# Optimization experiments

Measured on AMD Instinct MI355X. Metric: run time of the kernel, lower is better.

Reference implementation:

```python
import jax, jax.numpy as jnp
import numpy as np

B, C_IN, C_OUT, D, H, W = 2, 128, 128, 16, 32, 32


def setup_inputs() -> dict:
    key = jax.random.key(0)
    kx, kw, kb = jax.random.split(key, 3)
    x = jax.random.normal(kx, (B, C_IN, D, H, W), dtype=jnp.float32)
    # ddpm_conv3x3 -> Conv3d(in_ch, out_ch, kernel=3, padding=1) with default (scaled-variance) init
    fan_in = C_IN * 3 * 3 * 3
    scale = 1.0 / np.sqrt(fan_in)
    Wk = jax.random.uniform(kw, (C_OUT, C_IN, 3, 3, 3), dtype=jnp.float32, minval=-scale, maxval=scale)
    b = jnp.zeros((C_OUT,), dtype=jnp.float32)
    return {"x": x, "Wk": Wk, "b": b}


def reference(x, Wk, b):
    h = jnp.repeat(jnp.repeat(jnp.repeat(x, 2, axis=2), 2, axis=3), 2, axis=4)
    # 3x3x3 conv, stride 1, padding 1 (SAME)
    out = jax.lax.conv_general_dilated(
        h, Wk,
        window_strides=(1, 1, 1),
        padding="SAME",
        dimension_numbers=("NCDHW", "OIDHW", "NCDHW"),
    )
    return out + b[None, :, None, None, None]
```

## Files before the change

kernel.cpp:

```cpp
#include <hip/hip_runtime.h>
#include <hip/hip_bf16.h>

#define B_    2
#define CIN   128
#define COUT  128
#define DD    16
#define HH    32
#define WW    32
#define OS_H2 64
#define OS_D2 (64*64)
#define OS_CO (32*64*64)
#define OS_B  (COUT*OS_CO)

#define PD_D   18
#define PD_H   34
#define RD     17
#define RDB    68
#define HWDW   (PD_H*RD)
#define PLB    (HWDW*4)
#define CIW    (PD_D*HWDW)
#define CIB    (CIW*4)
#define CI8B   (8*CIB)
#define ARRD   ((size_t)B_*CIN*CIW)
#define ARRB   (ARRD*4)
#define AFOLD_BYTES (8*32*8*64*16)

typedef __attribute__((ext_vector_type(8))) short        short8;
typedef __attribute__((ext_vector_type(4))) float        floatx4;
typedef __attribute__((ext_vector_type(4))) unsigned int uint4v;

static __device__ __forceinline__ unsigned f2bf(float f) {
    union { __hip_bfloat16 h; unsigned short u; } cv;
    cv.h = __float2bfloat16(f);
    return (unsigned)cv.u;
}

__global__ __launch_bounds__(256) void fold_kernel(const float* __restrict__ Wk,
                                                   unsigned short* __restrict__ Afold) {
    const int t = blockIdx.x * 256 + threadIdx.x;
    const int p  = t >> 14;
    const int ks = (t >> 9) & 31;
    const int ct = (t >> 6) & 7;
    const int l  = t & 63;
    const int co = ct * 16 + (l & 15);
    const int ci = ks * 4 + (l >> 4);
    const int ed = (p >> 2) & 1, eh = (p >> 1) & 1, ew = p & 1;

    const float* w = Wk + (co * CIN + ci) * 27;
    float wv[27];
    #pragma unroll
    for (int i = 0; i < 27; ++i) wv[i] = w[i];

    short8 pk;
    #pragma unroll
    for (int tt = 0; tt < 8; ++tt) {
        const int td = (tt >> 2) & 1, th = (tt >> 1) & 1, tw = tt & 1;
        const int dlo = ed ? (td ? 2 : 0) : (td ? 1 : 0);
        const int dhi = ed ? (td ? 2 : 1) : (td ? 2 : 0);
        const int hlo = eh ? (th ? 2 : 0) : (th ? 1 : 0);
        const int hhi = eh ? (th ? 2 : 1) : (th ? 2 : 0);
        const int wlo = ew ? (tw ? 2 : 0) : (tw ? 1 : 0);
        const int whi = ew ? (tw ? 2 : 1) : (tw ? 2 : 0);
        float s = 0.f;
        for (int kd = dlo; kd <= dhi; ++kd)
            for (int kh = hlo; kh <= hhi; ++kh)
                for (int kw = wlo; kw <= whi; ++kw)
                    s += wv[kd * 9 + kh * 3 + kw];
        pk[tt] = (short)f2bf(s);
    }
    reinterpret_cast<short8*>(Afold)[t] = pk;
}

__global__ __launch_bounds__(256) void pad_kernel(const float* __restrict__ x,
                                                  unsigned* __restrict__ xe) {
    const int idx = blockIdx.x * 256 + threadIdx.x;
    const int w2 = idx & 15;
    const int h  = (idx >> 4) & 31;
    const int d  = (idx >> 9) & 15;
    const int ci = (idx >> 13) & 127;
    const int b  = (idx >> 20) & 1;
    const float2 v = *reinterpret_cast<const float2*>(
        x + (size_t)((b * CIN + ci) * DD + d) * (HH * WW) + h * WW + w2 * 2);
    xe[(size_t)((b * CIN + ci) * PD_D + d + 1) * HWDW
       + (h + 1) * RD + (w2 + 1)] = f2bf(v.x) | (f2bf(v.y) << 16);
}

__global__ __launch_bounds__(256) void xo_kernel(const unsigned* __restrict__ xe,
                                                 unsigned* __restrict__ xo) {
    const size_t t = (size_t)blockIdx.x * 256 + threadIdx.x;
    const unsigned e0 = xe[t];
    const unsigned e1 = (t + 1 < ARRD) ? xe[t + 1] : 0u;
    xo[t] = (e0 >> 16) | (e1 << 16);
}

__global__ __launch_bounds__(256, 3) void upconv_mfma(
    const char* __restrict__ xe_c, const char* __restrict__ xo_c,
    const unsigned short* __restrict__ Afold,
    const float* __restrict__ bias,
    float* __restrict__ out)
{
    __shared__ short Bt[2][128 * 64];
    char* buf0 = reinterpret_cast<char*>(&Bt[0][0]);
    char* buf1 = reinterpret_cast<char*>(&Bt[1][0]);

    const int tid  = threadIdx.x;
    const int wave = tid >> 6;
    const int lane = tid & 63;

    const int d      = blockIdx.x >> 3;
    const int h_base = (blockIdx.x & 7) * 4;
    const int p      = blockIdx.y;
    const int b      = blockIdx.z;
    const int ed = (p >> 2) & 1, eh = (p >> 1) & 1, ew = p & 1;

    const int npair = tid & 63;
    const int grp   = tid >> 6;
    const int hl    = npair >> 4;
    const int s     = npair & 15;
    const int n_a   = hl * 32 + 2 * s;
    const int n_b   = n_a + 1;
    const char* pa = ew ? xe_c : xo_c;
    const char* pb = ew ? xo_c : xe_c;
    const int dpad0 = d + ed;
    const int hpad0 = h_base + hl + eh;
    const long rowb = ((long)(b * CIN + grp * 2) * PD_D + dpad0) * (long)PLB
                    + (long)hpad0 * RDB;
    int offA[2], offB[2];
    offA[0] = (int)rowb + (s + ew) * 4;
    offB[0] = (int)rowb + (s + 1) * 4;
    offA[1] = offA[0] + CIB;
    offB[1] = offB[0] + CIB;

    int waddr_a[2], waddr_b[2];
    #pragma unroll
    for (int i = 0; i < 2; ++i) {
        const int cl = grp * 2 + i;
        waddr_a[i] = n_a * 128 + ((cl * 16) ^ (((n_a >> 1) & 7) << 4));
        waddr_b[i] = n_b * 128 + ((cl * 16) ^ (((n_b >> 1) & 7) << 4));
    }

    const int co0 = (wave >> 1) * 64;
    const int n0  = (wave & 1) * 64;
    const int ct0 = (wave >> 1) * 4;
    int raddr[2][4];
    #pragma unroll
    for (int ksl = 0; ksl < 2; ++ksl)
        #pragma unroll
        for (int nt = 0; nt < 4; ++nt) {
            const int n  = n0 + nt * 16 + (lane & 15);
            const int kb = ksl * 64 + (lane >> 4) * 16;
            raddr[ksl][nt] = n * 128 + (kb ^ (((n >> 1) & 7) << 4));
        }

    floatx4 acc[4][4];
    #pragma unroll
    for (int i = 0; i < 4; ++i)
        #pragma unroll
        for (int j = 0; j < 4; ++j)
            acc[i][j] = (floatx4){0.f, 0.f, 0.f, 0.f};

    const short8* Ap = reinterpret_cast<const short8*>(Afold);

    unsigned ga[2][4], gb[2][4];

    #define GATHER()                                                            \
        do {                                                                    \
            _Pragma("unroll")                                                   \
            for (int i = 0; i < 2; ++i) {                                       \
                const char* ba = pa + offA[i];                                  \
                const char* bb = pb + offB[i];                                  \
                ga[i][0] = *(const unsigned*)(ba + 0);                          \
                ga[i][1] = *(const unsigned*)(ba + RDB);                        \
                ga[i][2] = *(const unsigned*)(ba + PLB);                        \
                ga[i][3] = *(const unsigned*)(ba + PLB + RDB);                  \
                gb[i][0] = *(const unsigned*)(bb + 0);                          \
                gb[i][1] = *(const unsigned*)(bb + RDB);                        \
                gb[i][2] = *(const unsigned*)(bb + PLB);                        \
                gb[i][3] = *(const unsigned*)(bb + PLB + RDB);                  \
                offA[i] += CI8B; offB[i] += CI8B;                               \
            }                                                                   \
        } while (0)

    #define BODY(kc, bufc, dofill)                                              \
        do {                                                                    \
            short8 a[2][4];                                                     \
            _Pragma("unroll")                                                   \
            for (int ksl = 0; ksl < 2; ++ksl)                                   \
                _Pragma("unroll")                                               \
                for (int ct = 0; ct < 4; ++ct)                                  \
                    a[ksl][ct] = Ap[(size_t)(((p) * 32 + (kc) * 2 + ksl) * 8    \
                                             + ct0 + ct) * 64 + lane];          \
            _Pragma("unroll")                                                   \
            for (int i = 0; i < 2; ++i) {                                       \
                *(uint4v*)(bufc + waddr_a[i]) =                                 \
                    (uint4v){ga[i][0], ga[i][1], ga[i][2], ga[i][3]};           \
                *(uint4v*)(bufc + waddr_b[i]) =                                 \
                    (uint4v){gb[i][0], gb[i][1], gb[i][2], gb[i][3]};           \
            }                                                                   \
            if (dofill) GATHER();                                               \
            asm volatile("s_waitcnt lgkmcnt(0)\n\ts_barrier" ::: "memory");     \
            __builtin_amdgcn_s_setprio(1);                                      \
            _Pragma("unroll")                                                   \
            for (int ksl = 0; ksl < 2; ++ksl) {                                 \
                short8 bfr[4];                                                  \
                _Pragma("unroll")                                               \
                for (int nt = 0; nt < 4; ++nt)                                  \
                    bfr[nt] = *reinterpret_cast<const short8*>(                 \
                        (bufc) + raddr[ksl][nt]);                               \
                _Pragma("unroll")                                               \
                for (int ct = 0; ct < 4; ++ct)                                  \
                    _Pragma("unroll")                                           \
                    for (int nt = 0; nt < 4; ++nt)                              \
                        acc[ct][nt] = __builtin_amdgcn_mfma_f32_16x16x32_bf16(  \
                            a[ksl][ct], bfr[nt], acc[ct][nt], 0, 0, 0);         \
            }                                                                   \
            __builtin_amdgcn_s_setprio(0);                                      \
        } while (0)

    GATHER();
    for (int kc = 0; kc < 16; kc += 2) {
        BODY(kc,     buf0, true);
        BODY(kc + 1, buf1, (kc + 1) != 15);
    }
    #undef BODY
    #undef GATHER

    float* ob = out + (size_t)b * OS_B + (size_t)(2 * d + ed) * OS_D2;
    #pragma unroll
    for (int ct = 0; ct < 4; ++ct) {
        #pragma unroll
        for (int j = 0; j < 4; ++j) {
            const int co = co0 + ct * 16 + (lane >> 4) * 4 + j;
            const float bv = bias[co];
            #pragma unroll
            for (int nt = 0; nt < 4; ++nt) {
                const int n  = n0 + nt * 16 + (lane & 15);
                const int hh = n >> 5, wl = n & 31;
                const int h2 = 2 * (h_base + hh) + eh;
                const int w2 = 2 * wl + ew;
                ob[(size_t)co * OS_CO + h2 * OS_H2 + w2] = acc[ct][nt][j] + bv;
            }
        }
    }
}

extern "C" void kernel_launch(void* const* d_in, const int* in_sizes, int n_in,
                              void* d_out, int out_size, void* d_ws, size_t ws_size,
                              hipStream_t stream) {
    const float* x    = (const float*)d_in[0];
    const float* Wk   = (const float*)d_in[1];
    const float* bias = (const float*)d_in[2];
    float* out        = (float*)d_out;

    unsigned short* Afold = (unsigned short*)d_ws;
    char* xe = (char*)d_ws + AFOLD_BYTES;
    char* xo = xe + ARRB;

    hipMemsetAsync(xe, 0, ARRB, stream);
    pad_kernel<<<8192, 256, 0, stream>>>(x, (unsigned*)xe);
    xo_kernel<<<(unsigned)(ARRD / 256), 256, 0, stream>>>((const unsigned*)xe,
                                                          (unsigned*)xo);
    fold_kernel<<<512, 256, 0, stream>>>(Wk, Afold);

    dim3 grid(DD * 8, 8, B_);
    upconv_mfma<<<grid, 256, 0, stream>>>(xe, xo, Afold, bias, out);
}
```

Baseline: 115.9 us.

## Warp-specialize conv kernel with dedicated producer waves gathering into LDS

Adds two extra waves per block (384 threads) that only gather the padded bf16 input tiles from global memory and write them into the double-buffered LDS. The four MFMA waves now only prefetch weight fragments one step ahead and run matrix multiplies between barriers. The aim is to take global-gather latency and LDS-write work off the compute waves' critical path. In exchange the producer waves hold two in-flight gather sets, which raises register pressure and per-block resources. The barrier handshake between producer and consumer waves must also stay matched.

```diff
diff --git a/kernel.cpp b/kernel.cpp
--- a/kernel.cpp
+++ b/kernel.cpp
@@ -93,7 +93,7 @@
     xo[t] = (e0 >> 16) | (e1 << 16);
 }
 
-__global__ __launch_bounds__(256, 3) void upconv_mfma(
+__global__ __launch_bounds__(384, 3) void upconv_mfma(
     const char* __restrict__ xe_c, const char* __restrict__ xo_c,
     const unsigned short* __restrict__ Afold,
     const float* __restrict__ bias,
@@ -103,45 +103,90 @@
     char* buf0 = reinterpret_cast<char*>(&Bt[0][0]);
     char* buf1 = reinterpret_cast<char*>(&Bt[1][0]);
 
-    const int tid  = threadIdx.x;
-    const int wave = tid >> 6;
-    const int lane = tid & 63;
-
+    const int tid = threadIdx.x;
     const int d      = blockIdx.x >> 3;
     const int h_base = (blockIdx.x & 7) * 4;
     const int p      = blockIdx.y;
     const int b      = blockIdx.z;
     const int ed = (p >> 2) & 1, eh = (p >> 1) & 1, ew = p & 1;
 
-    const int npair = tid & 63;
-    const int grp   = tid >> 6;
-    const int hl    = npair >> 4;
-    const int s     = npair & 15;
-    const int n_a   = hl * 32 + 2 * s;
-    const int n_b   = n_a + 1;
-    const char* pa = ew ? xe_c : xo_c;
-    const char* pb = ew ? xo_c : xe_c;
-    const int dpad0 = d + ed;
-    const int hpad0 = h_base + hl + eh;
-    const long rowb = ((long)(b * CIN + grp * 2) * PD_D + dpad0) * (long)PLB
-                    + (long)hpad0 * RDB;
-    int offA[2], offB[2];
-    offA[0] = (int)rowb + (s + ew) * 4;
-    offB[0] = (int)rowb + (s + 1) * 4;
-    offA[1] = offA[0] + CIB;
-    offB[1] = offB[0] + CIB;
-
-    int waddr_a[2], waddr_b[2];
-    #pragma unroll
-    for (int i = 0; i < 2; ++i) {
-        const int cl = grp * 2 + i;
-        waddr_a[i] = n_a * 128 + ((cl * 16) ^ (((n_a >> 1) & 7) << 4));
-        waddr_b[i] = n_b * 128 + ((cl * 16) ^ (((n_b >> 1) & 7) << 4));
-    }
-
+    if (tid >= 256) {
+        const int ptid  = tid - 256;
+        const int npair = ptid & 63;
+        const int grp   = ptid >> 6;
+        const int hl    = npair >> 4;
+        const int s     = npair & 15;
+        const int n_a   = hl * 32 + 2 * s;
+        const int n_b   = n_a + 1;
+        const char* pa = ew ? xe_c : xo_c;
+        const char* pb = ew ? xo_c : xe_c;
+        const long rowb = ((long)(b * CIN + grp * 4) * PD_D + (d + ed)) * (long)PLB
+                        + (long)(h_base + hl + eh) * RDB;
+        int offA = (int)rowb + (s + ew) * 4;
+        int offB = (int)rowb + (s + 1) * 4;
+
+        int waddr_a[4], waddr_b[4];
+        #pragma unroll
+        for (int i = 0; i < 4; ++i) {
+            const int cl = grp * 4 + i;
+            waddr_a[i] = n_a * 128 + ((cl * 16) ^ (((n_a >> 1) & 7) << 4));
+            waddr_b[i] = n_b * 128 + ((cl * 16) ^ (((n_b >> 1) & 7) << 4));
+        }
+
+        unsigned gaA[4][4], gbA[4][4], gaB[4][4], gbB[4][4];
+
+        #define GATHERP(ga, gb)                                                 \
+            do {                                                                \
+                _Pragma("unroll")                                               \
+                for (int i = 0; i < 4; ++i) {                                   \
+                    const char* ba = pa + offA + i * CIB;                       \
+                    const char* bb = pb + offB + i * CIB;                       \
+                    ga[i][0] = *(const unsigned*)(ba + 0);                      \
+                    ga[i][1] = *(const unsigned*)(ba + RDB);                    \
+                    ga[i][2] = *(const unsigned*)(ba + PLB);                    \
+                    ga[i][3] = *(const unsigned*)(ba + PLB + RDB);              \
+                    gb[i][0] = *(const unsigned*)(bb + 0);                      \
+                    gb[i][1] = *(const unsigned*)(bb + RDB);                    \
+                    gb[i][2] = *(const unsigned*)(bb + PLB);                    \
+                    gb[i][3] = *(const unsigned*)(bb + PLB + RDB);              \
+                }                                                               \
+                offA += CI8B; offB += CI8B;                                     \
+            } while (0)
+
+        #define PWRITE(bufc, ga, gb)                                            \
+            do {                                                                \
+                _Pragma("unroll")                                               \
+                for (int i = 0; i < 4; ++i) {                                   \
+                    *(uint4v*)(bufc + waddr_a[i]) =                             \
+                        (uint4v){ga[i][0], ga[i][1], ga[i][2], ga[i][3]};       \
+                    *(uint4v*)(bufc + waddr_b[i]) =                             \
+                        (uint4v){gb[i][0], gb[i][1], gb[i][2], gb[i][3]};       \
+                }                                                               \
+            } while (0)
+
+        GATHERP(gaA, gbA);
+        GATHERP(gaB, gbB);
+        for (int kc = 0; kc < 16; kc += 2) {
+            PWRITE(buf0, gaA, gbA);
+            if (kc + 2 < 16) GATHERP(gaA, gbA);
+            asm volatile("s_waitcnt lgkmcnt(0)" ::: "memory");
+            __builtin_amdgcn_s_barrier();
+            PWRITE(buf1, gaB, gbB);
+            if (kc + 3 < 16) GATHERP(gaB, gbB);
+            asm volatile("s_waitcnt lgkmcnt(0)" ::: "memory");
+            __builtin_amdgcn_s_barrier();
+        }
+        #undef PWRITE
+        #undef GATHERP
+        return;
+    }
+
+    const int wave = tid >> 6;
+    const int lane = tid & 63;
     const int co0 = (wave >> 1) * 64;
     const int n0  = (wave & 1) * 64;
     const int ct0 = (wave >> 1) * 4;
+
     int raddr[2][4];
     #pragma unroll
     for (int ksl = 0; ksl < 2; ++ksl)
@@ -161,44 +206,20 @@
 
     const short8* Ap = reinterpret_cast<const short8*>(Afold);
 
-    unsigned ga[2][4], gb[2][4];
-
-    #define GATHER()                                                            \
+    short8 aC[2][4], aN[2][4];
+
+    #define ALOAD(a, kc)                                                        \
         do {                                                                    \
-            _Pragma("unroll")                                                   \
-            for (int i = 0; i < 2; ++i) {                                       \
-                const char* ba = pa + offA[i];                                  \
-                const char* bb = pb + offB[i];                                  \
-                ga[i][0] = *(const unsigned*)(ba + 0);                          \
-                ga[i][1] = *(const unsigned*)(ba + RDB);                        \
-                ga[i][2] = *(const unsigned*)(ba + PLB);                        \
-                ga[i][3] = *(const unsigned*)(ba + PLB + RDB);                  \
-                gb[i][0] = *(const unsigned*)(bb + 0);                          \
-                gb[i][1] = *(const unsigned*)(bb + RDB);                        \
-                gb[i][2] = *(const unsigned*)(bb + PLB);                        \
-                gb[i][3] = *(const unsigned*)(bb + PLB + RDB);                  \
-                offA[i] += CI8B; offB[i] += CI8B;                               \
-            }                                                                   \
-        } while (0)
-
-    #define BODY(kc, bufc, dofill)                                              \
-        do {                                                                    \
-            short8 a[2][4];                                                     \
             _Pragma("unroll")                                                   \
             for (int ksl = 0; ksl < 2; ++ksl)                                   \
                 _Pragma("unroll")                                               \
                 for (int ct = 0; ct < 4; ++ct)                                  \
                     a[ksl][ct] = Ap[(size_t)(((p) * 32 + (kc) * 2 + ksl) * 8    \
                                              + ct0 + ct) * 64 + lane];          \
-            _Pragma("unroll")                                                   \
-            for (int i = 0; i < 2; ++i) {                                       \
-                *(uint4v*)(bufc + waddr_a[i]) =                                 \
-                    (uint4v){ga[i][0], ga[i][1], ga[i][2], ga[i][3]};           \
-                *(uint4v*)(bufc + waddr_b[i]) =                                 \
-                    (uint4v){gb[i][0], gb[i][1], gb[i][2], gb[i][3]};           \
-            }                                                                   \
-            if (dofill) GATHER();                                               \
-            asm volatile("s_waitcnt lgkmcnt(0)\n\ts_barrier" ::: "memory");     \
+        } while (0)
+
+    #define MFMABLOCK(bufc, a)                                                  \
+        do {                                                                    \
             __builtin_amdgcn_s_setprio(1);                                      \
             _Pragma("unroll")                                                   \
             for (int ksl = 0; ksl < 2; ++ksl) {                                 \
@@ -217,13 +238,17 @@
             __builtin_amdgcn_s_setprio(0);                                      \
         } while (0)
 
-    GATHER();
+    ALOAD(aC, 0);
     for (int kc = 0; kc < 16; kc += 2) {
-        BODY(kc,     buf0, true);
-        BODY(kc + 1, buf1, (kc + 1) != 15);
-    }
-    #undef BODY
-    #undef GATHER
+        ALOAD(aN, kc + 1);
+        __builtin_amdgcn_s_barrier();
+        MFMABLOCK(buf0, aC);
+        if (kc + 2 < 16) ALOAD(aC, kc + 2);
+        __builtin_amdgcn_s_barrier();
+        MFMABLOCK(buf1, aN);
+    }
+    #undef MFMABLOCK
+    #undef ALOAD
 
     float* ob = out + (size_t)b * OS_B + (size_t)(2 * d + ed) * OS_D2;
     #pragma unroll
@@ -263,5 +288,5 @@
     fold_kernel<<<512, 256, 0, stream>>>(Wk, Afold);
 
     dim3 grid(DD * 8, 8, B_);
-    upconv_mfma<<<grid, 256, 0, stream>>>(xe, xo, Afold, bias, out);
-}
+    upconv_mfma<<<grid, 384, 0, stream>>>(xe, xo, Afold, bias, out);
+}
```

After: 182.0 us. +56.9%, slower.

## Double the spatial tile per block to reuse folded weights across more outputs

Applied to the files above, without the earlier changes.

Each block now covers 8 output rows (256 spatial positions) instead of 4. Each wave computes a 64x128 tile with 4x8 accumulators, so every A-fragment load from the folded weights serves twice as many MFMAs, and the grid is halved. In exchange, LDS per block doubles to 64KB, accumulator registers double, and launch bounds drop to 2 blocks per CU. The grid falls to 1024 blocks, which lowers occupancy and the scheduler's ability to hide latency.

```diff
diff --git a/kernel.cpp b/kernel.cpp
--- a/kernel.cpp
+++ b/kernel.cpp
@@ -93,13 +93,13 @@
     xo[t] = (e0 >> 16) | (e1 << 16);
 }
 
-__global__ __launch_bounds__(256, 3) void upconv_mfma(
+__global__ __launch_bounds__(256, 2) void upconv_mfma(
     const char* __restrict__ xe_c, const char* __restrict__ xo_c,
     const unsigned short* __restrict__ Afold,
     const float* __restrict__ bias,
     float* __restrict__ out)
 {
-    __shared__ short Bt[2][128 * 64];
+    __shared__ short Bt[2][256 * 64];
     char* buf0 = reinterpret_cast<char*>(&Bt[0][0]);
     char* buf1 = reinterpret_cast<char*>(&Bt[1][0]);
 
@@ -107,68 +107,63 @@
     const int wave = tid >> 6;
     const int lane = tid & 63;
 
-    const int d      = blockIdx.x >> 3;
-    const int h_base = (blockIdx.x & 7) * 4;
+    const int d      = blockIdx.x >> 2;
+    const int h_base = (blockIdx.x & 3) * 8;
     const int p      = blockIdx.y;
     const int b      = blockIdx.z;
     const int ed = (p >> 2) & 1, eh = (p >> 1) & 1, ew = p & 1;
 
-    const int npair = tid & 63;
-    const int grp   = tid >> 6;
+    const int npair = tid & 127;
+    const int cig   = tid >> 7;
     const int hl    = npair >> 4;
     const int s     = npair & 15;
     const int n_a   = hl * 32 + 2 * s;
     const int n_b   = n_a + 1;
     const char* pa = ew ? xe_c : xo_c;
     const char* pb = ew ? xo_c : xe_c;
-    const int dpad0 = d + ed;
-    const int hpad0 = h_base + hl + eh;
-    const long rowb = ((long)(b * CIN + grp * 2) * PD_D + dpad0) * (long)PLB
-                    + (long)hpad0 * RDB;
-    int offA[2], offB[2];
-    offA[0] = (int)rowb + (s + ew) * 4;
-    offB[0] = (int)rowb + (s + 1) * 4;
-    offA[1] = offA[0] + CIB;
-    offB[1] = offB[0] + CIB;
-
-    int waddr_a[2], waddr_b[2];
-    #pragma unroll
-    for (int i = 0; i < 2; ++i) {
-        const int cl = grp * 2 + i;
+    const long rowb = ((long)(b * CIN + cig * 4) * PD_D + (d + ed)) * (long)PLB
+                    + (long)(h_base + hl + eh) * RDB;
+    int offA = (int)rowb + (s + ew) * 4;
+    int offB = (int)rowb + (s + 1) * 4;
+
+    int waddr_a[4], waddr_b[4];
+    #pragma unroll
+    for (int i = 0; i < 4; ++i) {
+        const int cl = cig * 4 + i;
         waddr_a[i] = n_a * 128 + ((cl * 16) ^ (((n_a >> 1) & 7) << 4));
         waddr_b[i] = n_b * 128 + ((cl * 16) ^ (((n_b >> 1) & 7) << 4));
     }
 
-    const int co0 = (wave >> 1) * 64;
-    const int n0  = (wave & 1) * 64;
-    const int ct0 = (wave >> 1) * 4;
-    int raddr[2][4];
+    const int co0   = (wave >> 1) * 64;
+    const int nbase = (wave & 1) * 128;
+    const int ct0   = (wave >> 1) * 4;
+    int raddr[2][8];
     #pragma unroll
     for (int ksl = 0; ksl < 2; ++ksl)
         #pragma unroll
-        for (int nt = 0; nt < 4; ++nt) {
-            const int n  = n0 + nt * 16 + (lane & 15);
+        for (int nt = 0; nt < 8; ++nt) {
+            const int n  = nbase + nt * 16 + (lane & 15);
             const int kb = ksl * 64 + (lane >> 4) * 16;
             raddr[ksl][nt] = n * 128 + (kb ^ (((n >> 1) & 7) << 4));
         }
 
-    floatx4 acc[4][4];
+    floatx4 acc[4][8];
     #pragma unroll
     for (int i = 0; i < 4; ++i)
         #pragma unroll
-        for (int j = 0; j < 4; ++j)
+        for (int j = 0; j < 8; ++j)
             acc[i][j] = (floatx4){0.f, 0.f, 0.f, 0.f};
 
     const short8* Ap = reinterpret_cast<const short8*>(Afold);
 
-    unsigned ga[2][4], gb[2][4];
+    unsigned ga[4][4], gb[4][4];
 
     #define GATHER()                                                            \
         do {                                                                    \
             _Pragma("unroll")                                                   \
-            for (int i = 0; i < 2; ++i) {                                       \
-                const char* ba = pa + offA[i];                                  \
-                const char* bb = pb + offB[i];                                  \
+            for (int i = 0; i < 4; ++i) {                                       \
+                const char* ba = pa + offA + i * CIB;                           \
+                const char* bb = pb + offB + i * CIB;                           \
                 ga[i][0] = *(const unsigned*)(ba + 0);                          \
                 ga[i][1] = *(const unsigned*)(ba + RDB);                        \
                 ga[i][2] = *(const unsigned*)(ba + PLB);                        \
@@ -177,8 +172,8 @@
                 gb[i][1] = *(const unsigned*)(bb + RDB);                        \
                 gb[i][2] = *(const unsigned*)(bb + PLB);                        \
                 gb[i][3] = *(const unsigned*)(bb + PLB + RDB);                  \
-                offA[i] += CI8B; offB[i] += CI8B;                               \
             }                                                                   \
+            offA += CI8B; offB += CI8B;                                         \
         } while (0)
 
     #define BODY(kc, bufc, dofill)                                              \
@@ -191,7 +186,7 @@
                     a[ksl][ct] = Ap[(size_t)(((p) * 32 + (kc) * 2 + ksl) * 8    \
                                              + ct0 + ct) * 64 + lane];          \
             _Pragma("unroll")                                                   \
-            for (int i = 0; i < 2; ++i) {                                       \
+            for (int i = 0; i < 4; ++i) {                                       \
                 *(uint4v*)(bufc + waddr_a[i]) =                                 \
                     (uint4v){ga[i][0], ga[i][1], ga[i][2], ga[i][3]};           \
                 *(uint4v*)(bufc + waddr_b[i]) =                                 \
@@ -202,17 +197,15 @@
             __builtin_amdgcn_s_setprio(1);                                      \
             _Pragma("unroll")                                                   \
             for (int ksl = 0; ksl < 2; ++ksl) {                                 \
-                short8 bfr[4];                                                  \
                 _Pragma("unroll")                                               \
-                for (int nt = 0; nt < 4; ++nt)                                  \
-                    bfr[nt] = *reinterpret_cast<const short8*>(                 \
+                for (int nt = 0; nt < 8; ++nt) {                                \
+                    const short8 bfr = *reinterpret_cast<const short8*>(        \
                         (bufc) + raddr[ksl][nt]);                               \
-                _Pragma("unroll")                                               \
-                for (int ct = 0; ct < 4; ++ct)                                  \
                     _Pragma("unroll")                                           \
-                    for (int nt = 0; nt < 4; ++nt)                              \
+                    for (int ct = 0; ct < 4; ++ct)                              \
                         acc[ct][nt] = __builtin_amdgcn_mfma_f32_16x16x32_bf16(  \
-                            a[ksl][ct], bfr[nt], acc[ct][nt], 0, 0, 0);         \
+                            a[ksl][ct], bfr, acc[ct][nt], 0, 0, 0);             \
+                }                                                               \
             }                                                                   \
             __builtin_amdgcn_s_setprio(0);                                      \
         } while (0)
@@ -233,8 +226,8 @@
             const int co = co0 + ct * 16 + (lane >> 4) * 4 + j;
             const float bv = bias[co];
             #pragma unroll
-            for (int nt = 0; nt < 4; ++nt) {
-                const int n  = n0 + nt * 16 + (lane & 15);
+            for (int nt = 0; nt < 8; ++nt) {
+                const int n  = nbase + nt * 16 + (lane & 15);
                 const int hh = n >> 5, wl = n & 31;
                 const int h2 = 2 * (h_base + hh) + eh;
                 const int w2 = 2 * wl + ew;
@@ -262,6 +255,6 @@
                                                           (unsigned*)xo);
     fold_kernel<<<512, 256, 0, stream>>>(Wk, Afold);
 
-    dim3 grid(DD * 8, 8, B_);
+    dim3 grid(DD * 4, 8, B_);
     upconv_mfma<<<grid, 256, 0, stream>>>(xe, xo, Afold, bias, out);
 }
```

After: 125.9 us. +8.6%, slower.

## Load B fragments directly from global into registers, dropping LDS staging

Applied to the files above, without the earlier changes.

Removes the shared-memory staging buffer and barriers. Each lane now gathers its own MFMA B-operand fragment straight from the padded even/odd bf16 arrays into registers, with a two-deep register double buffer for both A and B. Occupancy drops from 3 to 2 blocks per SIMD target to make room for the extra registers. This avoids LDS writes, reads and workgroup syncs, but each wave now issues redundant global gathers (two waves share the same B data) and register pressure rises.

```diff
diff --git a/kernel.cpp b/kernel.cpp
--- a/kernel.cpp
+++ b/kernel.cpp
@@ -20,7 +20,6 @@
 #define PLB    (HWDW*4)
 #define CIW    (PD_D*HWDW)
 #define CIB    (CIW*4)
-#define CI8B   (8*CIB)
 #define ARRD   ((size_t)B_*CIN*CIW)
 #define ARRB   (ARRD*4)
 #define AFOLD_BYTES (8*32*8*64*16)
@@ -29,10 +28,10 @@
 typedef __attribute__((ext_vector_type(4))) float        floatx4;
 typedef __attribute__((ext_vector_type(4))) unsigned int uint4v;
 
-static __device__ __forceinline__ unsigned f2bf(float f) {
+static __device__ __forceinline__ unsigned short f2bf(float f) {
     union { __hip_bfloat16 h; unsigned short u; } cv;
     cv.h = __float2bfloat16(f);
-    return (unsigned)cv.u;
+    return cv.u;
 }
 
 __global__ __launch_bounds__(256) void fold_kernel(const float* __restrict__ Wk,
@@ -82,7 +81,7 @@
     const float2 v = *reinterpret_cast<const float2*>(
         x + (size_t)((b * CIN + ci) * DD + d) * (HH * WW) + h * WW + w2 * 2);
     xe[(size_t)((b * CIN + ci) * PD_D + d + 1) * HWDW
-       + (h + 1) * RD + (w2 + 1)] = f2bf(v.x) | (f2bf(v.y) << 16);
+       + (h + 1) * RD + (w2 + 1)] = (unsigned)f2bf(v.x) | ((unsigned)f2bf(v.y) << 16);
 }
 
 __global__ __launch_bounds__(256) void xo_kernel(const unsigned* __restrict__ xe,
@@ -93,16 +92,12 @@
     xo[t] = (e0 >> 16) | (e1 << 16);
 }
 
-__global__ __launch_bounds__(256, 3) void upconv_mfma(
+__global__ __launch_bounds__(256, 2) void upconv_mfma(
     const char* __restrict__ xe_c, const char* __restrict__ xo_c,
     const unsigned short* __restrict__ Afold,
     const float* __restrict__ bias,
     float* __restrict__ out)
 {
-    __shared__ short Bt[2][128 * 64];
-    char* buf0 = reinterpret_cast<char*>(&Bt[0][0]);
-    char* buf1 = reinterpret_cast<char*>(&Bt[1][0]);
-
     const int tid  = threadIdx.x;
     const int wave = tid >> 6;
     const int lane = tid & 63;
@@ -113,44 +108,18 @@
     const int b      = blockIdx.z;
     const int ed = (p >> 2) & 1, eh = (p >> 1) & 1, ew = p & 1;
 
-    const int npair = tid & 63;
-    const int grp   = tid >> 6;
-    const int hl    = npair >> 4;
-    const int s     = npair & 15;
-    const int n_a   = hl * 32 + 2 * s;
-    const int n_b   = n_a + 1;
-    const char* pa = ew ? xe_c : xo_c;
-    const char* pb = ew ? xo_c : xe_c;
-    const int dpad0 = d + ed;
-    const int hpad0 = h_base + hl + eh;
-    const long rowb = ((long)(b * CIN + grp * 2) * PD_D + dpad0) * (long)PLB
-                    + (long)hpad0 * RDB;
-    int offA[2], offB[2];
-    offA[0] = (int)rowb + (s + ew) * 4;
-    offB[0] = (int)rowb + (s + 1) * 4;
-    offA[1] = offA[0] + CIB;
-    offB[1] = offB[0] + CIB;
-
-    int waddr_a[2], waddr_b[2];
-    #pragma unroll
-    for (int i = 0; i < 2; ++i) {
-        const int cl = grp * 2 + i;
-        waddr_a[i] = n_a * 128 + ((cl * 16) ^ (((n_a >> 1) & 7) << 4));
-        waddr_b[i] = n_b * 128 + ((cl * 16) ^ (((n_b >> 1) & 7) << 4));
-    }
-
     const int co0 = (wave >> 1) * 64;
     const int n0  = (wave & 1) * 64;
     const int ct0 = (wave >> 1) * 4;
-    int raddr[2][4];
-    #pragma unroll
-    for (int ksl = 0; ksl < 2; ++ksl)
-        #pragma unroll
-        for (int nt = 0; nt < 4; ++nt) {
-            const int n  = n0 + nt * 16 + (lane & 15);
-            const int kb = ksl * 64 + (lane >> 4) * 16;
-            raddr[ksl][nt] = n * 128 + (kb ^ (((n >> 1) & 7) << 4));
-        }
+
+    const int lodd = lane & 1;
+    const char* arr = (ew != lodd) ? xe_c : xo_c;
+    const int ci_l  = lane >> 4;
+    const int col0  = ((lane & 15) >> 1) + (lodd ? 1 : ew);
+    const char* bbase = arr
+        + ((long)(b * CIN + ci_l) * PD_D + (d + ed)) * (long)PLB
+        + (long)(h_base + eh + (n0 >> 5)) * RDB
+        + (long)col0 * 4;
 
     floatx4 acc[4][4];
     #pragma unroll
@@ -161,69 +130,66 @@
 
     const short8* Ap = reinterpret_cast<const short8*>(Afold);
 
-    unsigned ga[2][4], gb[2][4];
-
-    #define GATHER()                                                            \
+    uint4v B0[2][4], B1[2][4];
+    short8 A0[2][4], A1[2][4];
+
+    #define LOADB(Bf, kc)                                                       \
         do {                                                                    \
             _Pragma("unroll")                                                   \
-            for (int i = 0; i < 2; ++i) {                                       \
-                const char* ba = pa + offA[i];                                  \
-                const char* bb = pb + offB[i];                                  \
-                ga[i][0] = *(const unsigned*)(ba + 0);                          \
-                ga[i][1] = *(const unsigned*)(ba + RDB);                        \
-                ga[i][2] = *(const unsigned*)(ba + PLB);                        \
-                ga[i][3] = *(const unsigned*)(ba + PLB + RDB);                  \
-                gb[i][0] = *(const unsigned*)(bb + 0);                          \
-                gb[i][1] = *(const unsigned*)(bb + RDB);                        \
-                gb[i][2] = *(const unsigned*)(bb + PLB);                        \
-                gb[i][3] = *(const unsigned*)(bb + PLB + RDB);                  \
-                offA[i] += CI8B; offB[i] += CI8B;                               \
-            }                                                                   \
+            for (int ksl = 0; ksl < 2; ++ksl)                                   \
+                _Pragma("unroll")                                               \
+                for (int nt = 0; nt < 4; ++nt) {                                \
+                    const char* fb = bbase + (long)((kc) * 8 + ksl * 4) * CIB   \
+                                   + (nt >> 1) * RDB + (nt & 1) * 32;           \
+                    Bf[ksl][nt] = (uint4v){                                     \
+                        *(const unsigned*)(fb),                                 \
+                        *(const unsigned*)(fb + RDB),                           \
+                        *(const unsigned*)(fb + PLB),                           \
+                        *(const unsigned*)(fb + PLB + RDB)};                    \
+                }                                                               \
         } while (0)
 
-    #define BODY(kc, bufc, dofill)                                              \
+    #define LOADA(Af, kc)                                                       \
         do {                                                                    \
-            short8 a[2][4];                                                     \
             _Pragma("unroll")                                                   \
             for (int ksl = 0; ksl < 2; ++ksl)                                   \
                 _Pragma("unroll")                                               \
                 for (int ct = 0; ct < 4; ++ct)                                  \
-                    a[ksl][ct] = Ap[(size_t)(((p) * 32 + (kc) * 2 + ksl) * 8    \
-                                             + ct0 + ct) * 64 + lane];          \
-            _Pragma("unroll")                                                   \
-            for (int i = 0; i < 2; ++i) {                                       \
-                *(uint4v*)(bufc + waddr_a[i]) =                                 \
-                    (uint4v){ga[i][0], ga[i][1], ga[i][2], ga[i][3]};           \
-                *(uint4v*)(bufc + waddr_b[i]) =                                 \
-                    (uint4v){gb[i][0], gb[i][1], gb[i][2], gb[i][3]};           \
-            }                                                                   \
-            if (dofill) GATHER();                                               \
-            asm volatile("s_waitcnt lgkmcnt(0)\n\ts_barrier" ::: "memory");     \
+                    Af[ksl][ct] = Ap[(size_t)(((p) * 32 + (kc) * 2 + ksl) * 8   \
+                                              + ct0 + ct) * 64 + lane];         \
+        } while (0)
+
+    #define MFMAC(Af, Bf)                                                       \
+        do {                                                                    \
             __builtin_amdgcn_s_setprio(1);                                      \
             _Pragma("unroll")                                                   \
-            for (int ksl = 0; ksl < 2; ++ksl) {                                 \
-                short8 bfr[4];                                                  \
+            for (int ksl = 0; ksl < 2; ++ksl)                                   \
                 _Pragma("unroll")                                               \
-                for (int nt = 0; nt < 4; ++nt)                                  \
-                    bfr[nt] = *reinterpret_cast<const short8*>(                 \
-                        (bufc) + raddr[ksl][nt]);                               \
-                _Pragma("unroll")                                               \
-                for (int ct = 0; ct < 4; ++ct)                                  \
+                for (int nt = 0; nt < 4; ++nt) {                                \
+                    const short8 bfr = __builtin_bit_cast(short8, Bf[ksl][nt]); \
                     _Pragma("unroll")                                           \
-                    for (int nt = 0; nt < 4; ++nt)                              \
+                    for (int ct = 0; ct < 4; ++ct)                              \
                         acc[ct][nt] = __builtin_amdgcn_mfma_f32_16x16x32_bf16(  \
-                            a[ksl][ct], bfr[nt], acc[ct][nt], 0, 0, 0);         \
-            }                                                                   \
+                            Af[ksl][ct], bfr, acc[ct][nt], 0, 0, 0);            \
+                }                                                               \
             __builtin_amdgcn_s_setprio(0);                                      \
         } while (0)
 
-    GATHER();
+    LOADB(B0, 0);
+    LOADA(A0, 0);
     for (int kc = 0; kc < 16; kc += 2) {
-        BODY(kc,     buf0, true);
-        BODY(kc + 1, buf1, (kc + 1) != 15);
+        LOADB(B1, kc + 1);
+        LOADA(A1, kc + 1);
+        MFMAC(A0, B0);
+        if (kc + 2 < 16) {
+            LOADB(B0, kc + 2);
+            LOADA(A0, kc + 2);
+        }
+        MFMAC(A1, B1);
     }
-    #undef BODY
-    #undef GATHER
+    #undef MFMAC
+    #undef LOADA
+    #undef LOADB
 
     float* ob = out + (size_t)b * OS_B + (size_t)(2 * d + ed) * OS_D2;
     #pragma unroll
```

After: 174.1 us. 1.5x slower.
